# Kernel optimization log

Measured on AMD Instinct MI355X. Metric: run time of the kernel, lower is better.

## Reference

```python
import jax, jax.numpy as jnp
import numpy as np

K_SIZE = 3            # kernel_size
PAD = K_SIZE // 2     # zero padding on each side
EPS = 1e-5            # torch layer_norm default eps


def setup_inputs() -> dict:
    key = jax.random.key(0)
    ks = jax.random.split(key, 9)
    B, C, H, W = 4, 256, 64, 64
    Cout = 256
    sc = 1.0 / np.sqrt(C)
    return {
        "x":  jax.random.normal(ks[0], (B, C, H, W), dtype=jnp.float32),
        "Wq": jax.random.normal(ks[1], (C, C), dtype=jnp.float32) * sc,
        "bq": jax.random.normal(ks[2], (C,), dtype=jnp.float32) * 0.02,
        "Wk": jax.random.normal(ks[3], (C, C), dtype=jnp.float32) * sc,
        "bk": jax.random.normal(ks[4], (C,), dtype=jnp.float32) * 0.02,
        "Wv": jax.random.normal(ks[5], (C, C), dtype=jnp.float32) * sc,
        "bv": jax.random.normal(ks[6], (C,), dtype=jnp.float32) * 0.02,
        "Wo": jax.random.normal(ks[7], (C, Cout), dtype=jnp.float32) * sc,
        "bo": jax.random.normal(ks[8], (Cout,), dtype=jnp.float32) * 0.02,
    }


def _forward(x, Wq, bq, Wk, bk, Wv, bv, Wo, bo):
    B, C, H, W = x.shape
    # F.layer_norm(x, [H, W]): normalize over last two dims per (b, c), no affine
    mean = jnp.mean(x, axis=(2, 3), keepdims=True)
    var = jnp.var(x, axis=(2, 3), keepdims=True)
    xn = (x - mean) * jax.lax.rsqrt(var + EPS)
    # zero pad spatial dims
    p = jnp.pad(xn, ((0, 0), (0, 0), (PAD, PAD), (PAD, PAD)))
    # channels-last for per-pixel linears
    p = jnp.transpose(p, (0, 2, 3, 1))          # [B, Hp, Wp, C]
    xc = jnp.transpose(xn, (0, 2, 3, 1))        # [B, H,  W,  C] (window centers)
    scale = jnp.asarray(C, x.dtype) ** -0.5     # depth_scale = C**-0.5
    q = (xc @ Wq + bq) * scale                  # [B, H, W, C] (center-token query)
    kf = p @ Wk + bk                            # [B, Hp, Wp, C]
    vf = p @ Wv + bv
    # gather the kk=9 shifted views -> window tokens per pixel
    Kw = jnp.stack([kf[:, dh:dh + H, dw:dw + W, :]
                    for dh in range(K_SIZE) for dw in range(K_SIZE)], axis=3)  # [B,H,W,kk,C]
    Vw = jnp.stack([vf[:, dh:dh + H, dw:dw + W, :]
                    for dh in range(K_SIZE) for dw in range(K_SIZE)], axis=3)
    logits = jnp.einsum('bhwc,bhwnc->bhwn', q, Kw)     # [B, H, W, kk]
    attn = jax.nn.softmax(logits, axis=-1)
    ctx = jnp.einsum('bhwn,bhwnc->bhwc', attn, Vw)     # [B, H, W, C]
    out = ctx @ Wo + bo                                # [B, H, W, Cout]
    return jnp.transpose(out, (0, 3, 1, 2))            # [B, Cout, H, W]


def reference(x, Wq, bq, Wk, bk, Wv, bv, Wo, bo):
    return _forward(x, Wq, bq, Wk, bk, Wv, bv, Wo, bo)
```

## Files before the change

### kernel.cpp

```cpp
#include <hip/hip_runtime.h>
#include <hip/hip_bf16.h>
#include <stdint.h>

typedef __bf16 bf16x8 __attribute__((ext_vector_type(8)));
typedef float f32x4 __attribute__((ext_vector_type(4)));

#define KDIM 256
#define M_PAD 17536
#define NPIX 16384
#define QKVS 768

__device__ __forceinline__ float b2f(ushort u){
    union { float f; uint32_t i; } x; x.i = ((uint32_t)u) << 16; return x.f;
}
__device__ __forceinline__ ushort f2b(float f){
    uint32_t u = __float_as_uint(f);
    uint32_t r = (u + 0x7fffu + ((u >> 16) & 1u)) >> 16;
    return (ushort)r;
}

__global__ __launch_bounds__(256)
void prep(const float* __restrict__ x,
          const float* __restrict__ Wq, const float* __restrict__ bq,
          const float* __restrict__ Wk, const float* __restrict__ bk,
          const float* __restrict__ Wv, const float* __restrict__ bv,
          const float* __restrict__ Wo,
          ushort* __restrict__ wt, float* __restrict__ bias_all,
          float* __restrict__ mean, float* __restrict__ rstd,
          ushort* __restrict__ xn){
    __shared__ float sh[32 * 33];
    const int bid = blockIdx.x, tid = threadIdx.x;

    if (bid < 1024){
        int bc = bid;
        const float4* p = (const float4*)(x + (size_t)bc * 4096);
        float s = 0.f, s2 = 0.f;
#pragma unroll
        for (int i = 0; i < 4; ++i){
            float4 v = p[i * 256 + tid];
            s  += v.x + v.y + v.z + v.w;
            s2 += v.x * v.x + v.y * v.y + v.z * v.z + v.w * v.w;
        }
#pragma unroll
        for (int off = 32; off; off >>= 1){
            s  += __shfl_xor(s, off);
            s2 += __shfl_xor(s2, off);
        }
        int wid = tid >> 6;
        if ((tid & 63) == 0){ sh[wid] = s; sh[4 + wid] = s2; }
        __syncthreads();
        if (tid == 0){
            float S  = sh[0] + sh[1] + sh[2] + sh[3];
            float S2 = sh[4] + sh[5] + sh[6] + sh[7];
            float m  = S * (1.f / 4096.f);
            float v  = S2 * (1.f / 4096.f) - m * m;
            mean[bc] = m;
            rstd[bc] = rsqrtf(v + 1e-5f);
        }
    } else if (bid < 1280){
        int t = bid - 1024;
        int m = t >> 6, tile = t & 63;
        int ti = tile & 7, tj = tile >> 3;
        const float* src = (m == 0) ? Wq : (m == 1) ? Wk : (m == 2) ? Wv : Wo;
        float scale = (m == 0) ? 0.0625f : 1.0f;
        int roff = m * 256;
        int tx = tid & 31, ty = tid >> 5;
#pragma unroll
        for (int i = 0; i < 4; ++i){
            int sr = tj * 32 + ty + i * 8;
            sh[(ty + i * 8) * 33 + tx] = src[sr * 256 + ti * 32 + tx] * scale;
        }
        __syncthreads();
#pragma unroll
        for (int i = 0; i < 4; ++i){
            int dr = ti * 32 + ty + i * 8;
            wt[(size_t)(roff + dr) * 256 + tj * 32 + tx] =
                f2b(sh[tx * 33 + ty + i * 8]);
        }
    } else if (bid == 1280){
        bias_all[tid]       = bq[tid] * 0.0625f;
        bias_all[256 + tid] = bk[tid];
        bias_all[512 + tid] = bv[tid];
    } else {
        int p = (bid - 1281) * 8 + (tid >> 5);
        int row;
        if (p < 1040){
            int b = p / 260, i = p % 260;
            int h, w;
            if (i < 66)       { h = 0;       w = i; }
            else if (i < 132) { h = 65;      w = i - 66; }
            else if (i < 196) { h = i - 131; w = 0; }
            else              { h = i - 195; w = 65; }
            row = b * 4356 + h * 66 + w;
        } else {
            row = 17424 + (p - 1040);
        }
        uint4 z = {0, 0, 0, 0};
        *(uint4*)(xn + (size_t)row * 256 + (tid & 31) * 8) = z;
    }
}

__global__ void ln_apply(const float* __restrict__ x, const float* __restrict__ mean,
                         const float* __restrict__ rstd, ushort* __restrict__ xn){
    int blk = blockIdx.x;
    int b = blk >> 6, h = blk & 63;
    int c = threadIdx.x;
    int bc = b * 256 + c;
    float mu = mean[bc], rv = rstd[bc];
    const float* px = x + ((size_t)bc * 64 + h) * 64;
    ushort* po = xn + (((size_t)(b * 66 + h + 1) * 66) + 1) * 256 + c;
#pragma unroll 4
    for (int w = 0; w < 64; ++w)
        po[(size_t)w * 256] = f2b((px[w] - mu) * rv);
}

template<int MODE, int NOUT>
__global__ __launch_bounds__(256, 2)
void gemm_nt(const ushort* __restrict__ X, const ushort* __restrict__ Y,
             const float* __restrict__ bias,
             ushort* __restrict__ zb, float* __restrict__ zf){
    __shared__ ushort ldsX[2][128 * 64];
    __shared__ ushort ldsY[2][128 * 64];
    const int tid  = threadIdx.x;
    const int lane = tid & 63;
    const int wid  = tid >> 6;
    const int wm   = wid >> 1, wn = wid & 1;
    const int x0   = blockIdx.x * 128, y0 = blockIdx.y * 128;

    auto stage = [&](int buf, int k0){
#pragma unroll
        for (int i = 0; i < 4; ++i){
            int f   = i * 256 + tid;
            int row = f >> 3, cp = f & 7;
            int cs  = cp ^ (row & 7);
            const ushort* gx = X + (size_t)(x0 + row) * KDIM + k0 + cs * 8;
            const ushort* gy = Y + (size_t)(y0 + row) * KDIM + k0 + cs * 8;
            __builtin_amdgcn_global_load_lds(
                (const __attribute__((address_space(1))) void*)gx,
                (__attribute__((address_space(3))) void*)&ldsX[buf][f * 8], 16, 0, 0);
            __builtin_amdgcn_global_load_lds(
                (const __attribute__((address_space(1))) void*)gy,
                (__attribute__((address_space(3))) void*)&ldsY[buf][f * 8], 16, 0, 0);
        }
    };

    f32x4 acc[4][4];
#pragma unroll
    for (int i = 0; i < 4; ++i)
#pragma unroll
        for (int j = 0; j < 4; ++j) acc[i][j] = f32x4{0.f, 0.f, 0.f, 0.f};

    stage(0, 0);
    int buf = 0;
    for (int t = 0; t < 4; ++t){
        __syncthreads();
        if (t < 3) stage(buf ^ 1, (t + 1) * 64);
#pragma unroll
        for (int kk = 0; kk < 2; ++kk){
            bf16x8 xa[4], yb[4];
#pragma unroll
            for (int fm = 0; fm < 4; ++fm){
                int r = wm * 64 + fm * 16 + (lane & 15);
                int c = kk * 4 + (lane >> 4);
                xa[fm] = *(const bf16x8*)&ldsX[buf][(r * 8 + (c ^ (r & 7))) * 8];
            }
#pragma unroll
            for (int fn = 0; fn < 4; ++fn){
                int r = wn * 64 + fn * 16 + (lane & 15);
                int c = kk * 4 + (lane >> 4);
                yb[fn] = *(const bf16x8*)&ldsY[buf][(r * 8 + (c ^ (r & 7))) * 8];
            }
#pragma unroll
            for (int fm = 0; fm < 4; ++fm)
#pragma unroll
                for (int fn = 0; fn < 4; ++fn)
                    acc[fm][fn] = __builtin_amdgcn_mfma_f32_16x16x32_bf16(
                        xa[fm], yb[fn], acc[fm][fn], 0, 0, 0);
        }
        buf ^= 1;
    }

#pragma unroll
    for (int fm = 0; fm < 4; ++fm){
#pragma unroll
        for (int fn = 0; fn < 4; ++fn){
            int xr = x0 + wm * 64 + fm * 16 + ((lane >> 4) << 2);
            int yc = y0 + wn * 64 + fn * 16 + (lane & 15);
            if (MODE == 0){
                float bv = bias[yc];
#pragma unroll
                for (int r = 0; r < 4; ++r)
                    zb[(size_t)(xr + r) * NOUT + yc] = f2b(acc[fm][fn][r] + bv);
            } else {
                int bpix = yc >> 12, hw = yc & 4095;
#pragma unroll
                for (int r = 0; r < 4; ++r){
                    int ch = xr + r;
                    zf[((size_t)(bpix * 256 + ch)) * 4096 + hw] =
                        acc[fm][fn][r] + bias[ch];
                }
            }
        }
    }
}

__global__ __launch_bounds__(256)
void attn_win(const ushort* __restrict__ qkv, ushort* __restrict__ ctx){
    int pix  = blockIdx.x * 4 + (threadIdx.x >> 6);
    int lane = threadIdx.x & 63;
    int b = pix >> 12, hw = pix & 4095;
    int h = hw >> 6, w = hw & 63;
    size_t base = (size_t)b * 66 * 66;
    size_t crow = base + (size_t)(h + 1) * 66 + (w + 1);

    ushort4 q4 = *(const ushort4*)(qkv + crow * QKVS + lane * 4);
    float q0 = b2f(q4.x), q1 = b2f(q4.y), q2 = b2f(q4.z), q3 = b2f(q4.w);

    float lg[9];
    size_t rows[9];
#pragma unroll
    for (int n = 0; n < 9; ++n){
        int dh = n / 3, dw = n % 3;
        size_t row = base + (size_t)(h + dh) * 66 + (w + dw);
        rows[n] = row;
        ushort4 k4 = *(const ushort4*)(qkv + row * QKVS + 256 + lane * 4);
        float d = q0 * b2f(k4.x) + q1 * b2f(k4.y) + q2 * b2f(k4.z) + q3 * b2f(k4.w);
#pragma unroll
        for (int off = 32; off; off >>= 1) d += __shfl_xor(d, off);
        lg[n] = d;
    }
    float m = lg[0];
#pragma unroll
    for (int n = 1; n < 9; ++n) m = fmaxf(m, lg[n]);
    float e[9], s = 0.f;
#pragma unroll
    for (int n = 0; n < 9; ++n){ e[n] = __expf(lg[n] - m); s += e[n]; }
    float inv = 1.f / s;

    float c0 = 0.f, c1 = 0.f, c2 = 0.f, c3 = 0.f;
#pragma unroll
    for (int n = 0; n < 9; ++n){
        float a = e[n] * inv;
        ushort4 v4 = *(const ushort4*)(qkv + rows[n] * QKVS + 512 + lane * 4);
        c0 += a * b2f(v4.x); c1 += a * b2f(v4.y);
        c2 += a * b2f(v4.z); c3 += a * b2f(v4.w);
    }
    ushort4 o; o.x = f2b(c0); o.y = f2b(c1); o.z = f2b(c2); o.w = f2b(c3);
    *(ushort4*)(ctx + (size_t)pix * 256 + lane * 4) = o;
}

extern "C" void kernel_launch(void* const* d_in, const int* in_sizes, int n_in,
                              void* d_out, int out_size, void* d_ws, size_t ws_size,
                              hipStream_t stream){
    const float* x  = (const float*)d_in[0];
    const float* Wq = (const float*)d_in[1];
    const float* bq = (const float*)d_in[2];
    const float* Wk = (const float*)d_in[3];
    const float* bk = (const float*)d_in[4];
    const float* Wv = (const float*)d_in[5];
    const float* bv = (const float*)d_in[6];
    const float* Wo = (const float*)d_in[7];
    const float* bo = (const float*)d_in[8];
    float* out = (float*)d_out;

    char* ws = (char*)d_ws;
    ushort* wt       = (ushort*)(ws);
    float*  bias_all = (float*) (ws + 524288);
    float*  mean     = (float*) (ws + 528384);
    float*  rstd     = (float*) (ws + 532480);
    ushort* xn       = (ushort*)(ws + 536576);
    ushort* qkv      = (ushort*)(ws + 9515008);
    ushort* ctx      = (ushort*)(ws + 36450304);

    prep<<<1425, 256, 0, stream>>>(x, Wq, bq, Wk, bk, Wv, bv, Wo,
                                   wt, bias_all, mean, rstd, xn);
    ln_apply<<<256, 256, 0, stream>>>(x, mean, rstd, xn);

    dim3 g1(137, 6);
    gemm_nt<0, QKVS><<<g1, 256, 0, stream>>>(xn, wt, bias_all, qkv, nullptr);

    attn_win<<<4096, 256, 0, stream>>>(qkv, ctx);

    dim3 g2(2, 128);
    gemm_nt<1, 0><<<g2, 256, 0, stream>>>(wt + 768 * 256, ctx, bo, nullptr, out);
}
```

Before: 58.09 us.

## Fold layer-norm scaling into per-batch QKV weights and bias, single pass over x

Reads x only once: a fused kernel transposes raw x to bf16 channels-last and accumulates partial sums. Instead of normalizing activations, the per-batch rstd is folded into per-batch copies of Wq/Wk/Wv and the mean term is folded into a per-batch bias. Padding rows are filled with the per-channel mean so they normalize to zero. This removes the separate stats read of x and the normalization pass, at the cost of extra small kernels, per-batch weight copies, padding each batch to a 128-row multiple, and precision risk from casting un-normalized x to bf16 before normalization.

```diff
diff --git a/kernel.cpp b/kernel.cpp
--- a/kernel.cpp
+++ b/kernel.cpp
@@ -6,7 +6,8 @@
 typedef float f32x4 __attribute__((ext_vector_type(4)));
 
 #define KDIM 256
-#define M_PAD 17536
+#define MB 4480
+#define MTOT 17920
 #define NPIX 16384
 #define QKVS 768
 
@@ -20,101 +21,130 @@
 }
 
 __global__ __launch_bounds__(256)
-void prep(const float* __restrict__ x,
-          const float* __restrict__ Wq, const float* __restrict__ bq,
-          const float* __restrict__ Wk, const float* __restrict__ bk,
-          const float* __restrict__ Wv, const float* __restrict__ bv,
-          const float* __restrict__ Wo,
-          ushort* __restrict__ wt, float* __restrict__ bias_all,
-          float* __restrict__ mean, float* __restrict__ rstd,
-          ushort* __restrict__ xn){
+void ln_fuse(const float* __restrict__ x, ushort* __restrict__ xt,
+             float* __restrict__ psum, float* __restrict__ psum2){
+    __shared__ ushort sh[256 * 68];
+    const int bid = blockIdx.x;
+    const int b = bid >> 6, h = bid & 63;
+    const int tid = threadIdx.x;
+    const float* xb = x + (size_t)b * 256 * 4096 + h * 64;
+    const int csub = tid >> 4, w4 = tid & 15;
+#pragma unroll
+    for (int i = 0; i < 16; ++i){
+        int c = i * 16 + csub;
+        float4 v = *(const float4*)(xb + (size_t)c * 4096 + w4 * 4);
+        ushort4 u; u.x = f2b(v.x); u.y = f2b(v.y); u.z = f2b(v.z); u.w = f2b(v.w);
+        *(ushort4*)&sh[c * 68 + w4 * 4] = u;
+    }
+    __syncthreads();
+    float s = 0.f, s2 = 0.f;
+    size_t rowbase = ((size_t)b * MB + (size_t)(h + 1) * 66 + 1) * 256;
+#pragma unroll 8
+    for (int w = 0; w < 64; ++w){
+        ushort u = sh[tid * 68 + w];
+        float f = b2f(u);
+        s += f; s2 += f * f;
+        xt[rowbase + (size_t)w * 256 + tid] = u;
+    }
+    psum [bid * 256 + tid] = s;
+    psum2[bid * 256 + tid] = s2;
+}
+
+__global__ __launch_bounds__(256)
+void stats_fin(const float* __restrict__ psum, const float* __restrict__ psum2,
+               float* __restrict__ rstd_g, float* __restrict__ mrv_g,
+               ushort* __restrict__ mb_g){
+    int b = blockIdx.x, tid = threadIdx.x;
+    float S = 0.f, S2 = 0.f;
+    for (int h = 0; h < 64; ++h){
+        S  += psum [(b * 64 + h) * 256 + tid];
+        S2 += psum2[(b * 64 + h) * 256 + tid];
+    }
+    float m  = S * (1.f / 4096.f);
+    float v  = S2 * (1.f / 4096.f) - m * m;
+    float rv = rsqrtf(v + 1e-5f);
+    rstd_g[b * 256 + tid] = rv;
+    mrv_g [b * 256 + tid] = m * rv;
+    mb_g  [b * 256 + tid] = f2b(m);
+}
+
+__global__ __launch_bounds__(256)
+void prep2(const float* __restrict__ Wq, const float* __restrict__ bq,
+           const float* __restrict__ Wk, const float* __restrict__ bk,
+           const float* __restrict__ Wv, const float* __restrict__ bv,
+           const float* __restrict__ Wo,
+           const float* __restrict__ rstd_g, const float* __restrict__ mrv_g,
+           const ushort* __restrict__ mb_g,
+           ushort* __restrict__ wtq, ushort* __restrict__ wot,
+           float* __restrict__ biasp, ushort* __restrict__ xt){
     __shared__ float sh[32 * 33];
     const int bid = blockIdx.x, tid = threadIdx.x;
-
-    if (bid < 1024){
-        int bc = bid;
-        const float4* p = (const float4*)(x + (size_t)bc * 4096);
-        float s = 0.f, s2 = 0.f;
-#pragma unroll
-        for (int i = 0; i < 4; ++i){
-            float4 v = p[i * 256 + tid];
-            s  += v.x + v.y + v.z + v.w;
-            s2 += v.x * v.x + v.y * v.y + v.z * v.z + v.w * v.w;
-        }
-#pragma unroll
-        for (int off = 32; off; off >>= 1){
-            s  += __shfl_xor(s, off);
-            s2 += __shfl_xor(s2, off);
-        }
-        int wid = tid >> 6;
-        if ((tid & 63) == 0){ sh[wid] = s; sh[4 + wid] = s2; }
+    if (bid < 192){
+        int mat = bid / 64, tile = bid % 64;
+        int ti = tile & 7, tj = tile >> 3;
+        const float* src = (mat == 0) ? Wq : (mat == 1) ? Wk : Wv;
+        float qs = (mat == 0) ? 0.0625f : 1.0f;
+        int tx = tid & 31, ty = tid >> 5;
+#pragma unroll
+        for (int i = 0; i < 4; ++i)
+            sh[(ty + i * 8) * 33 + tx] =
+                src[(size_t)(tj * 32 + ty + i * 8) * 256 + ti * 32 + tx] * qs;
         __syncthreads();
-        if (tid == 0){
-            float S  = sh[0] + sh[1] + sh[2] + sh[3];
-            float S2 = sh[4] + sh[5] + sh[6] + sh[7];
-            float m  = S * (1.f / 4096.f);
-            float v  = S2 * (1.f / 4096.f) - m * m;
-            mean[bc] = m;
-            rstd[bc] = rsqrtf(v + 1e-5f);
-        }
-    } else if (bid < 1280){
-        int t = bid - 1024;
-        int m = t >> 6, tile = t & 63;
+        int k = tj * 32 + tx;
+#pragma unroll
+        for (int b = 0; b < 4; ++b){
+            float rv = rstd_g[b * 256 + k];
+#pragma unroll
+            for (int i = 0; i < 4; ++i){
+                int n = mat * 256 + ti * 32 + ty + i * 8;
+                wtq[((size_t)b * 768 + n) * 256 + k] =
+                    f2b(sh[tx * 33 + ty + i * 8] * rv);
+            }
+        }
+    } else if (bid < 256){
+        int tile = bid - 192;
         int ti = tile & 7, tj = tile >> 3;
-        const float* src = (m == 0) ? Wq : (m == 1) ? Wk : (m == 2) ? Wv : Wo;
-        float scale = (m == 0) ? 0.0625f : 1.0f;
-        int roff = m * 256;
         int tx = tid & 31, ty = tid >> 5;
 #pragma unroll
-        for (int i = 0; i < 4; ++i){
-            int sr = tj * 32 + ty + i * 8;
-            sh[(ty + i * 8) * 33 + tx] = src[sr * 256 + ti * 32 + tx] * scale;
-        }
+        for (int i = 0; i < 4; ++i)
+            sh[(ty + i * 8) * 33 + tx] =
+                Wo[(size_t)(tj * 32 + ty + i * 8) * 256 + ti * 32 + tx];
         __syncthreads();
 #pragma unroll
-        for (int i = 0; i < 4; ++i){
-            int dr = ti * 32 + ty + i * 8;
-            wt[(size_t)(roff + dr) * 256 + tj * 32 + tx] =
+        for (int i = 0; i < 4; ++i)
+            wot[(size_t)(ti * 32 + ty + i * 8) * 256 + tj * 32 + tx] =
                 f2b(sh[tx * 33 + ty + i * 8]);
-        }
-    } else if (bid == 1280){
-        bias_all[tid]       = bq[tid] * 0.0625f;
-        bias_all[256 + tid] = bk[tid];
-        bias_all[512 + tid] = bv[tid];
+    } else if (bid < 268){
+        int t = bid - 256;
+        int b = t / 3, mat = t % 3;
+        const float* W  = (mat == 0) ? Wq : (mat == 1) ? Wk : Wv;
+        const float* bb = (mat == 0) ? bq : (mat == 1) ? bk : bv;
+        float qs = (mat == 0) ? 0.0625f : 1.0f;
+        float acc = 0.f;
+        for (int c = 0; c < 256; ++c)
+            acc += mrv_g[b * 256 + c] * W[(size_t)c * 256 + tid];
+        biasp[b * 768 + mat * 256 + tid] = (bb[tid] - acc) * qs;
     } else {
-        int p = (bid - 1281) * 8 + (tid >> 5);
-        int row;
-        if (p < 1040){
-            int b = p / 260, i = p % 260;
-            int h, w;
-            if (i < 66)       { h = 0;       w = i; }
-            else if (i < 132) { h = 65;      w = i - 66; }
-            else if (i < 196) { h = i - 131; w = 0; }
-            else              { h = i - 195; w = 65; }
-            row = b * 4356 + h * 66 + w;
-        } else {
-            row = 17424 + (p - 1040);
-        }
-        uint4 z = {0, 0, 0, 0};
-        *(uint4*)(xn + (size_t)row * 256 + (tid & 31) * 8) = z;
-    }
-}
-
-__global__ void ln_apply(const float* __restrict__ x, const float* __restrict__ mean,
-                         const float* __restrict__ rstd, ushort* __restrict__ xn){
-    int blk = blockIdx.x;
-    int b = blk >> 6, h = blk & 63;
-    int c = threadIdx.x;
-    int bc = b * 256 + c;
-    float mu = mean[bc], rv = rstd[bc];
-    const float* px = x + ((size_t)bc * 64 + h) * 64;
-    ushort* po = xn + (((size_t)(b * 66 + h + 1) * 66) + 1) * 256 + c;
-#pragma unroll 4
-    for (int w = 0; w < 64; ++w)
-        po[(size_t)w * 256] = f2b((px[w] - mu) * rv);
-}
-
-template<int MODE, int NOUT>
+        int t = bid - 268;
+        int b = t / 12, seg = t % 12;
+        ushort mb = mb_g[b * 256 + tid];
+        for (int r = 0; r < 32; ++r){
+            int j = seg * 32 + r;
+            int row;
+            if (j < 260){
+                int h66, w66;
+                if (j < 66)       { h66 = 0;       w66 = j; }
+                else if (j < 132) { h66 = 65;      w66 = j - 66; }
+                else if (j < 196) { h66 = j - 131; w66 = 0; }
+                else              { h66 = j - 195; w66 = 65; }
+                row = h66 * 66 + w66;
+            } else row = 4356 + (j - 260);
+            xt[((size_t)b * MB + row) * 256 + tid] = mb;
+        }
+    }
+}
+
+template<int MODE>
 __global__ __launch_bounds__(256, 2)
 void gemm_nt(const ushort* __restrict__ X, const ushort* __restrict__ Y,
              const float* __restrict__ bias,
@@ -126,6 +156,9 @@
     const int wid  = tid >> 6;
     const int wm   = wid >> 1, wn = wid & 1;
     const int x0   = blockIdx.x * 128, y0 = blockIdx.y * 128;
+    const int bsel = (MODE == 0) ? (x0 / MB) : 0;
+    const ushort* Yb   = (MODE == 0) ? Y + (size_t)bsel * 768 * 256 : Y;
+    const float* biasb = (MODE == 0) ? bias + bsel * 768 : bias;
 
     auto stage = [&](int buf, int k0){
 #pragma unroll
@@ -133,8 +166,8 @@
             int f   = i * 256 + tid;
             int row = f >> 3, cp = f & 7;
             int cs  = cp ^ (row & 7);
-            const ushort* gx = X + (size_t)(x0 + row) * KDIM + k0 + cs * 8;
-            const ushort* gy = Y + (size_t)(y0 + row) * KDIM + k0 + cs * 8;
+            const ushort* gx = X  + (size_t)(x0 + row) * KDIM + k0 + cs * 8;
+            const ushort* gy = Yb + (size_t)(y0 + row) * KDIM + k0 + cs * 8;
             __builtin_amdgcn_global_load_lds(
                 (const __attribute__((address_space(1))) void*)gx,
                 (__attribute__((address_space(3))) void*)&ldsX[buf][f * 8], 16, 0, 0);
@@ -187,10 +220,10 @@
             int xr = x0 + wm * 64 + fm * 16 + ((lane >> 4) << 2);
             int yc = y0 + wn * 64 + fn * 16 + (lane & 15);
             if (MODE == 0){
-                float bv = bias[yc];
+                float bv = biasb[yc];
 #pragma unroll
                 for (int r = 0; r < 4; ++r)
-                    zb[(size_t)(xr + r) * NOUT + yc] = f2b(acc[fm][fn][r] + bv);
+                    zb[(size_t)(xr + r) * QKVS + yc] = f2b(acc[fm][fn][r] + bv);
             } else {
                 int bpix = yc >> 12, hw = yc & 4095;
 #pragma unroll
@@ -210,7 +243,7 @@
     int lane = threadIdx.x & 63;
     int b = pix >> 12, hw = pix & 4095;
     int h = hw >> 6, w = hw & 63;
-    size_t base = (size_t)b * 66 * 66;
+    size_t base = (size_t)b * MB;
     size_t crow = base + (size_t)(h + 1) * 66 + (w + 1);
 
     ushort4 q4 = *(const ushort4*)(qkv + crow * QKVS + lane * 4);
@@ -264,23 +297,28 @@
     float* out = (float*)d_out;
 
     char* ws = (char*)d_ws;
-    ushort* wt       = (ushort*)(ws);
-    float*  bias_all = (float*) (ws + 524288);
-    float*  mean     = (float*) (ws + 528384);
-    float*  rstd     = (float*) (ws + 532480);
-    ushort* xn       = (ushort*)(ws + 536576);
-    ushort* qkv      = (ushort*)(ws + 9515008);
-    ushort* ctx      = (ushort*)(ws + 36450304);
-
-    prep<<<1425, 256, 0, stream>>>(x, Wq, bq, Wk, bk, Wv, bv, Wo,
-                                   wt, bias_all, mean, rstd, xn);
-    ln_apply<<<256, 256, 0, stream>>>(x, mean, rstd, xn);
-
-    dim3 g1(137, 6);
-    gemm_nt<0, QKVS><<<g1, 256, 0, stream>>>(xn, wt, bias_all, qkv, nullptr);
+    ushort* wtq    = (ushort*)(ws);
+    ushort* wot    = (ushort*)(ws + 1572864);
+    float*  biasp  = (float*) (ws + 1703936);
+    float*  psum   = (float*) (ws + 1716224);
+    float*  psum2  = (float*) (ws + 1978368);
+    float*  rstd_g = (float*) (ws + 2240512);
+    float*  mrv_g  = (float*) (ws + 2244608);
+    ushort* mb_g   = (ushort*)(ws + 2248704);
+    ushort* xt     = (ushort*)(ws + 2250752);
+    ushort* qkv    = (ushort*)(ws + 11425792);
+    ushort* ctx    = (ushort*)(ws + 38950912);
+
+    ln_fuse<<<256, 256, 0, stream>>>(x, xt, psum, psum2);
+    stats_fin<<<4, 256, 0, stream>>>(psum, psum2, rstd_g, mrv_g, mb_g);
+    prep2<<<316, 256, 0, stream>>>(Wq, bq, Wk, bk, Wv, bv, Wo,
+                                   rstd_g, mrv_g, mb_g, wtq, wot, biasp, xt);
+
+    dim3 g1(140, 6);
+    gemm_nt<0><<<g1, 256, 0, stream>>>(xt, wtq, biasp, qkv, nullptr);
 
     attn_win<<<4096, 256, 0, stream>>>(qkv, ctx);
 
     dim3 g2(2, 128);
-    gemm_nt<1, 0><<<g2, 256, 0, stream>>>(wt + 768 * 256, ctx, bo, nullptr, out);
-}
+    gemm_nt<1><<<g2, 256, 0, stream>>>(wot, ctx, bo, nullptr, out);
+}
```

Result: slower. 69.85 us (+20.2%).
